# Optimization experiments

Measured on AMD Instinct MI355X. Metric: run time of the kernel, lower is better.

The kernel has to match this reference:

```python
import jax, jax.numpy as jnp
import numpy as np

D_MODEL = 1024
HEADS = 16


def setup_inputs() -> dict:
    key = jax.random.key(0)
    ks = jax.random.split(key, 11)
    B, S, D = 2, 2048, D_MODEL
    scale = 1.0 / np.sqrt(D)
    inp = {
        "q": jax.random.normal(ks[0], (B, S, D), jnp.float32),
        "k": jax.random.normal(ks[1], (B, S, D), jnp.float32),
        "v": jax.random.normal(ks[2], (B, S, D), jnp.float32),
        "w_q": jax.random.normal(ks[3], (D, D), jnp.float32) * scale,
        "b_q": jnp.zeros((D,), jnp.float32),
        "w_k": jax.random.normal(ks[4], (D, D), jnp.float32) * scale,
        "b_k": jnp.zeros((D,), jnp.float32),
        "w_v": jax.random.normal(ks[5], (D, D), jnp.float32) * scale,
        "b_v": jnp.zeros((D,), jnp.float32),
        "w_o": jax.random.normal(ks[6], (D, D), jnp.float32) * scale,
        "b_o": jnp.zeros((D,), jnp.float32),
    }
    return inp


def reference(q, k, v, w_q, b_q, w_k, b_k, w_v, b_v, w_o, b_o):
    B, S, D = q.shape
    H = HEADS
    Dh = D // H

    def split(x):  # [B,S,D] -> [B,H,S,Dh]
        return x.reshape(B, S, H, Dh).transpose(0, 2, 1, 3)

    qh = split(q @ w_q + b_q)
    kh = split(k @ w_k + b_k)
    vh = split(v @ w_v + b_v)

    # scaled dot-product attention: softmax(Q K^T / sqrt(Dh)) V
    scores = jnp.einsum("bhsd,bhtd->bhst", qh, kh) / jnp.sqrt(
        jnp.asarray(Dh, qh.dtype)
    )
    attn = jax.nn.softmax(scores, axis=-1)
    out = jnp.einsum("bhst,bhtd->bhsd", attn, vh)

    concat = out.transpose(0, 2, 1, 3).reshape(B, S, D)
    return concat @ w_o + b_o
```

## Files before the change

### kernel.cpp

```cpp
#include <hip/hip_runtime.h>
#include <hip/hip_bf16.h>
#include <math.h>

using bf16 = __hip_bfloat16;
typedef __bf16 bf16x8v __attribute__((ext_vector_type(8)));
typedef float f32x4v __attribute__((ext_vector_type(4)));

#define AS1 __attribute__((address_space(1)))
#define AS3 __attribute__((address_space(3)))

__device__ __forceinline__ void g2l16(const void* g, void* l) {
  __builtin_amdgcn_global_load_lds((const AS1 void*)g, (AS3 void*)l, 16, 0, 0);
}

__device__ __forceinline__ float fclamp(float v) {
  return fminf(fmaxf(v, -6.0e4f), 6.0e4f);
}

__device__ __forceinline__ unsigned packbf(float a, float b) {
  unsigned short lo = __builtin_bit_cast(unsigned short, __float2bfloat16(a));
  unsigned short hi = __builtin_bit_cast(unsigned short, __float2bfloat16(b));
  return (unsigned)lo | ((unsigned)hi << 16);
}

#define QSCL 0.1803368801111204f

__global__ __launch_bounds__(256) void transpose_cvt4(
    const float* __restrict__ w0, const float* __restrict__ w1,
    const float* __restrict__ w2, const float* __restrict__ w3,
    bf16* __restrict__ o0, bf16* __restrict__ o1,
    bf16* __restrict__ o2, bf16* __restrict__ o3) {
  const float* in = (blockIdx.z == 0) ? w0 : (blockIdx.z == 1) ? w1
                    : (blockIdx.z == 2) ? w2 : w3;
  bf16* out = (blockIdx.z == 0) ? o0 : (blockIdx.z == 1) ? o1
              : (blockIdx.z == 2) ? o2 : o3;
  __shared__ alignas(16) bf16 tile[64][80];
  const int t = threadIdx.x;
  const int bx = blockIdx.x * 64, by = blockIdx.y * 64;
#pragma unroll
  for (int p = 0; p < 4; ++p) {
    int idx = p * 1024 + t * 4;
    int r = idx >> 6, c0 = idx & 63;
    float4 v = *(const float4*)&in[(size_t)(by + r) * 1024 + bx + c0];
    tile[c0 + 0][r] = __float2bfloat16(v.x);
    tile[c0 + 1][r] = __float2bfloat16(v.y);
    tile[c0 + 2][r] = __float2bfloat16(v.z);
    tile[c0 + 3][r] = __float2bfloat16(v.w);
  }
  __syncthreads();
#pragma unroll
  for (int p = 0; p < 2; ++p) {
    int idx = p * 2048 + t * 8;
    int c = idx >> 6, r0 = idx & 63;
    *(uint4*)&out[(size_t)(bx + c) * 1024 + by + r0] = *(const uint4*)&tile[c][r0];
  }
}

__global__ __launch_bounds__(256) void cvt3(
    const float* __restrict__ q, const float* __restrict__ k,
    const float* __restrict__ v, bf16* __restrict__ oq,
    bf16* __restrict__ ok, bf16* __restrict__ ov) {
  const float* in = (blockIdx.y == 0) ? q : (blockIdx.y == 1) ? k : v;
  bf16* out = (blockIdx.y == 0) ? oq : (blockIdx.y == 1) ? ok : ov;
  int i = (blockIdx.x * 256 + threadIdx.x) * 8;
  float4 a = *(const float4*)&in[i];
  float4 b = *(const float4*)&in[i + 4];
  uint4 u;
  u.x = packbf(a.x, a.y); u.y = packbf(a.z, a.w);
  u.z = packbf(b.x, b.y); u.w = packbf(b.z, b.w);
  *(uint4*)&out[i] = u;
}

__global__ __launch_bounds__(256, 2) void gemm_qkv_bf16(
    const bf16* __restrict__ Aq, const bf16* __restrict__ Ak,
    const bf16* __restrict__ Av,
    const bf16* __restrict__ WtQ, const bf16* __restrict__ WtK,
    const bf16* __restrict__ WtV,
    const float* __restrict__ bq, const float* __restrict__ bk_,
    const float* __restrict__ bv_,
    bf16* __restrict__ Qh, bf16* __restrict__ Kh, bf16* __restrict__ Vt) {
  constexpr int K = 1024;
  const int z = blockIdx.z;
  const bf16* A    = (z == 0) ? Aq : (z == 1) ? Ak : Av;
  const bf16* Bt   = (z == 0) ? WtQ : (z == 1) ? WtK : WtV;
  const float* bias = (z == 0) ? bq : (z == 1) ? bk_ : bv_;
  bf16* C = (z == 0) ? Qh : (z == 1) ? Kh : Vt;

  __shared__ alignas(16) bf16 As[3][128 * 32];
  __shared__ alignas(16) bf16 Bs[3][128 * 32];
  const int t = threadIdx.x;
  const int wave = t >> 6, lane = t & 63;
  const int quad = lane >> 4, l16 = lane & 15;
  const int bm = blockIdx.x * 128, bn = blockIdx.y * 128;
  const int wm = (wave & 1) * 64, wn = (wave >> 1) * 64;

  f32x4v acc[4][4] = {};

  auto stage = [&](int ks, int buf) {
    int k0 = ks * 32;
#pragma unroll
    for (int c = 0; c < 2; ++c) {
      int idx = c * 2048 + t * 8;
      int row = idx >> 5, col = idx & 31;
      g2l16(&A[(size_t)(bm + row) * K + k0 + col], &As[buf][c * 2048 + wave * 512]);
      g2l16(&Bt[(size_t)(bn + row) * K + k0 + col], &Bs[buf][c * 2048 + wave * 512]);
    }
  };

  auto compute = [&](int buf) {
    bf16x8v a[4], b[4];
#pragma unroll
    for (int mi = 0; mi < 4; ++mi)
      a[mi] = *(const bf16x8v*)&As[buf][(wm + mi * 16 + l16) * 32 + quad * 8];
#pragma unroll
    for (int ni = 0; ni < 4; ++ni)
      b[ni] = *(const bf16x8v*)&Bs[buf][(wn + ni * 16 + l16) * 32 + quad * 8];
#pragma unroll
    for (int mi = 0; mi < 4; ++mi)
#pragma unroll
      for (int ni = 0; ni < 4; ++ni)
        acc[mi][ni] = __builtin_amdgcn_mfma_f32_16x16x32_bf16(a[mi], b[ni],
                                                              acc[mi][ni], 0, 0, 0);
  };

  stage(0, 0);
  asm volatile("s_waitcnt vmcnt(0)" ::: "memory");
  __builtin_amdgcn_s_barrier();
  stage(1, 1);

  int bufc = 0;
  for (int tt = 0; tt < 30; ++tt) {
    int bufs = bufc + 2; if (bufs >= 3) bufs -= 3;
    stage(tt + 2, bufs);
    compute(bufc);
    asm volatile("s_waitcnt vmcnt(4)" ::: "memory");
    __builtin_amdgcn_s_barrier();
    bufc = (bufc == 2) ? 0 : bufc + 1;
  }
  compute(bufc);
  asm volatile("s_waitcnt vmcnt(0)" ::: "memory");
  __builtin_amdgcn_s_barrier();
  bufc = (bufc == 2) ? 0 : bufc + 1;
  compute(bufc);

  if (z == 2) {
#pragma unroll
    for (int ni = 0; ni < 4; ++ni) {
      int n = bn + wn + ni * 16 + l16;
      float bz = bias[n];
      int h_ = n >> 6, d_ = n & 63;
#pragma unroll
      for (int mi = 0; mi < 4; ++mi) {
        int m0 = bm + wm + mi * 16 + quad * 4;
        int b_ = m0 >> 11, s0 = m0 & 2047;
        uint2 u;
        u.x = packbf(fclamp(acc[mi][ni][0] + bz), fclamp(acc[mi][ni][1] + bz));
        u.y = packbf(fclamp(acc[mi][ni][2] + bz), fclamp(acc[mi][ni][3] + bz));
        *(uint2*)&C[((size_t)(b_ * 16 + h_) * 64 + d_) * 2048 + s0] = u;
      }
    }
  } else {
    const float scl = (z == 0) ? QSCL : 1.0f;
#pragma unroll
    for (int ni = 0; ni < 4; ++ni) {
      int n = bn + wn + ni * 16 + l16;
      float bz = bias[n];
      int h_ = n >> 6, d_ = n & 63;
#pragma unroll
      for (int mi = 0; mi < 4; ++mi)
#pragma unroll
        for (int r = 0; r < 4; ++r) {
          int m = bm + wm + mi * 16 + quad * 4 + r;
          int b_ = m >> 11, s_ = m & 2047;
          C[((size_t)(b_ * 16 + h_) * 2048 + s_) * 64 + d_] =
              __float2bfloat16(fclamp(acc[mi][ni][r] + bz) * scl);
        }
    }
  }
}

__global__ __launch_bounds__(256, 2) void gemm_out(
    const bf16* __restrict__ A, const bf16* __restrict__ Bt,
    const float* __restrict__ bias, float* __restrict__ C) {
  constexpr int K = 1024, N = 1024;
  __shared__ alignas(16) bf16 As[3][128 * 32];
  __shared__ alignas(16) bf16 Bs[3][64 * 32];
  const int t = threadIdx.x;
  const int wave = t >> 6, lane = t & 63;
  const int quad = lane >> 4, l16 = lane & 15;
  const int bm = blockIdx.x * 128, bn = blockIdx.y * 64;
  const int wm = (wave & 1) * 64, wn = (wave >> 1) * 32;

  f32x4v acc[4][2] = {};

  auto stage = [&](int ks, int buf) {
    int k0 = ks * 32;
#pragma unroll
    for (int c = 0; c < 2; ++c) {
      int idx = c * 2048 + t * 8;
      int row = idx >> 5, col = idx & 31;
      g2l16(&A[(size_t)(bm + row) * K + k0 + col], &As[buf][c * 2048 + wave * 512]);
    }
    {
      int idx = t * 8;
      int row = idx >> 5, col = idx & 31;
      g2l16(&Bt[(size_t)(bn + row) * K + k0 + col], &Bs[buf][wave * 512]);
    }
  };

  auto compute = [&](int buf) {
    bf16x8v a[4], b[2];
#pragma unroll
    for (int mi = 0; mi < 4; ++mi)
      a[mi] = *(const bf16x8v*)&As[buf][(wm + mi * 16 + l16) * 32 + quad * 8];
#pragma unroll
    for (int ni = 0; ni < 2; ++ni)
      b[ni] = *(const bf16x8v*)&Bs[buf][(wn + ni * 16 + l16) * 32 + quad * 8];
#pragma unroll
    for (int mi = 0; mi < 4; ++mi)
#pragma unroll
      for (int ni = 0; ni < 2; ++ni)
        acc[mi][ni] = __builtin_amdgcn_mfma_f32_16x16x32_bf16(a[mi], b[ni],
                                                              acc[mi][ni], 0, 0, 0);
  };

  stage(0, 0);
  asm volatile("s_waitcnt vmcnt(0)" ::: "memory");
  __builtin_amdgcn_s_barrier();
  stage(1, 1);

  int bufc = 0;
  for (int tt = 0; tt < 30; ++tt) {
    int bufs = bufc + 2; if (bufs >= 3) bufs -= 3;
    stage(tt + 2, bufs);
    compute(bufc);
    asm volatile("s_waitcnt vmcnt(3)" ::: "memory");
    __builtin_amdgcn_s_barrier();
    bufc = (bufc == 2) ? 0 : bufc + 1;
  }
  compute(bufc);
  asm volatile("s_waitcnt vmcnt(0)" ::: "memory");
  __builtin_amdgcn_s_barrier();
  bufc = (bufc == 2) ? 0 : bufc + 1;
  compute(bufc);

#pragma unroll
  for (int ni = 0; ni < 2; ++ni) {
    int n = bn + wn + ni * 16 + l16;
    float bz = bias[n];
#pragma unroll
    for (int mi = 0; mi < 4; ++mi)
#pragma unroll
      for (int r = 0; r < 4; ++r) {
        int m = bm + wm + mi * 16 + quad * 4 + r;
        C[(size_t)m * N + n] = fclamp(acc[mi][ni][r] + bz);
      }
  }
}

__global__ __launch_bounds__(512, 4) void attn(
    const bf16* __restrict__ Qh, const bf16* __restrict__ Kh,
    const bf16* __restrict__ Vt, bf16* __restrict__ Ctx) {
  constexpr int LDPP = 40;
  __shared__ alignas(16) bf16 QsPs[128 * 64];
  __shared__ alignas(16) bf16 Ks[3][64 * 64];
  __shared__ alignas(16) bf16 Vs[3][64 * 64];
  const int t = threadIdx.x;
  const int wave = t >> 6, lane = t & 63;
  const int quad = lane >> 4, l16 = lane & 15;
  const int sw = l16 & 7;

  const int lin = blockIdx.x;
  const int li = lin >> 3;
  const int qb = li & 15;
  const int bh = (lin & 7) * 4 + (li >> 4);

  const size_t bh_off = (size_t)bh * 2048 * 64;
  const bf16* Qb = Qh + bh_off;
  const bf16* Kb = Kh + bh_off;
  const bf16* Vb = Vt + bh_off;

  const int srow = t >> 3;
  const int schunk = t & 7;

  auto stageKV = [&](int kt, int buf) {
    int mc = schunk ^ (srow & 7);
    g2l16(&Kb[(size_t)(kt * 64 + srow) * 64 + mc * 8], &Ks[buf][wave * 512]);
    g2l16(&Vb[(size_t)srow * 2048 + kt * 64 + mc * 8], &Vs[buf][wave * 512]);
  };

#pragma unroll
  for (int c = 0; c < 2; ++c) {
    int row = c * 64 + srow;
    int mc = schunk ^ (row & 7);
    g2l16(&Qb[(size_t)(qb * 128 + row) * 64 + mc * 8],
          &QsPs[c * 4096 + wave * 512]);
  }
  stageKV(0, 0);
  asm volatile("s_waitcnt vmcnt(2)" ::: "memory");
  __builtin_amdgcn_s_barrier();

  bf16x8v aq[2];
#pragma unroll
  for (int kk = 0; kk < 2; ++kk)
    aq[kk] = *(const bf16x8v*)
        &QsPs[(wave * 16 + l16) * 64 + (((kk * 4 + quad) ^ sw) << 3)];

  __syncthreads();
  bf16* Psw = QsPs + wave * (16 * LDPP);

  stageKV(1, 1);

  bf16x8v vone;
#pragma unroll
  for (int i = 0; i < 8; ++i) vone[i] = (__bf16)1.0f;

  f32x4v lsum = {};
  f32x4v oacc[4] = {};

  auto compute = [&](int buf) {
#pragma unroll
    for (int h = 0; h < 2; ++h) {
      f32x4v s[2] = {};
      __builtin_amdgcn_s_setprio(1);
#pragma unroll
      for (int kk = 0; kk < 2; ++kk)
#pragma unroll
        for (int ni = 0; ni < 2; ++ni) {
          bf16x8v bk = *(const bf16x8v*)
              &Ks[buf][(h * 32 + ni * 16 + l16) * 64 + (((kk * 4 + quad) ^ sw) << 3)];
          s[ni] = __builtin_amdgcn_mfma_f32_16x16x32_bf16(bk, aq[kk],
                                                          s[ni], 0, 0, 0);
        }
      __builtin_amdgcn_s_setprio(0);

#pragma unroll
      for (int ni = 0; ni < 2; ++ni) {
        float p0 = __builtin_amdgcn_exp2f(fminf(s[ni][0], 80.f));
        float p1 = __builtin_amdgcn_exp2f(fminf(s[ni][1], 80.f));
        float p2 = __builtin_amdgcn_exp2f(fminf(s[ni][2], 80.f));
        float p3 = __builtin_amdgcn_exp2f(fminf(s[ni][3], 80.f));
        uint2 u;
        u.x = packbf(p0, p1);
        u.y = packbf(p2, p3);
        *(uint2*)&Psw[l16 * LDPP + ni * 16 + quad * 4] = u;
      }

      bf16x8v ap = *(const bf16x8v*)&Psw[l16 * LDPP + quad * 8];
      __builtin_amdgcn_s_setprio(1);
      lsum = __builtin_amdgcn_mfma_f32_16x16x32_bf16(ap, vone, lsum, 0, 0, 0);
#pragma unroll
      for (int ni = 0; ni < 4; ++ni) {
        bf16x8v bv = *(const bf16x8v*)
            &Vs[buf][(ni * 16 + l16) * 64 + (((h * 4 + quad) ^ sw) << 3)];
        oacc[ni] = __builtin_amdgcn_mfma_f32_16x16x32_bf16(ap, bv, oacc[ni],
                                                           0, 0, 0);
      }
      __builtin_amdgcn_s_setprio(0);
    }
  };

  int bufc = 0;
  for (int tt = 0; tt < 30; ++tt) {
    int bufs = bufc + 2; if (bufs >= 3) bufs -= 3;
    stageKV(tt + 2, bufs);
    compute(bufc);
    asm volatile("s_waitcnt vmcnt(2)" ::: "memory");
    __builtin_amdgcn_s_barrier();
    bufc = (bufc == 2) ? 0 : bufc + 1;
  }
  compute(bufc);
  asm volatile("s_waitcnt vmcnt(0)" ::: "memory");
  __builtin_amdgcn_s_barrier();
  bufc = (bufc == 2) ? 0 : bufc + 1;
  compute(bufc);

  const int b_ = bh >> 4, h_ = bh & 15;
#pragma unroll
  for (int r = 0; r < 4; ++r) {
    int sr = qb * 128 + wave * 16 + quad * 4 + r;
    float inv = 1.0f / fmaxf(lsum[r], 1.0e-20f);
#pragma unroll
    for (int ni = 0; ni < 4; ++ni) {
      int col = h_ * 64 + ni * 16 + l16;
      Ctx[(size_t)(b_ * 2048 + sr) * 1024 + col] =
          __float2bfloat16(fclamp(oacc[ni][r] * inv));
    }
  }
}

extern "C" void kernel_launch(void* const* d_in, const int* in_sizes, int n_in,
                              void* d_out, int out_size, void* d_ws, size_t ws_size,
                              hipStream_t stream) {
  const float* q   = (const float*)d_in[0];
  const float* k   = (const float*)d_in[1];
  const float* v   = (const float*)d_in[2];
  const float* w_q = (const float*)d_in[3];
  const float* b_q = (const float*)d_in[4];
  const float* w_k = (const float*)d_in[5];
  const float* b_k = (const float*)d_in[6];
  const float* w_v = (const float*)d_in[7];
  const float* b_v = (const float*)d_in[8];
  const float* w_o = (const float*)d_in[9];
  const float* b_o = (const float*)d_in[10];
  float* out = (float*)d_out;

  char* ws = (char*)d_ws;
  const size_t MB = (size_t)1024 * 1024;
  bf16* WtQ = (bf16*)(ws + 0 * MB);
  bf16* WtK = (bf16*)(ws + 2 * MB);
  bf16* WtV = (bf16*)(ws + 4 * MB);
  bf16* WtO = (bf16*)(ws + 6 * MB);
  bf16* Qa  = (bf16*)(ws + 8 * MB);
  bf16* Ka  = (bf16*)(ws + 16 * MB);
  bf16* Va  = (bf16*)(ws + 24 * MB);
  bf16* Qh  = (bf16*)(ws + 32 * MB);
  bf16* Kh  = (bf16*)(ws + 40 * MB);
  bf16* Vt  = (bf16*)(ws + 48 * MB);
  bf16* Ctx = Qa;

  dim3 tb(256);
  transpose_cvt4<<<dim3(16, 16, 4), tb, 0, stream>>>(w_q, w_k, w_v, w_o,
                                                     WtQ, WtK, WtV, WtO);
  cvt3<<<dim3(2048, 3), tb, 0, stream>>>(q, k, v, Qa, Ka, Va);
  gemm_qkv_bf16<<<dim3(32, 8, 3), tb, 0, stream>>>(Qa, Ka, Va, WtQ, WtK, WtV,
                                                   b_q, b_k, b_v, Qh, Kh, Vt);
  attn<<<dim3(512), dim3(512), 0, stream>>>(Qh, Kh, Vt, Ctx);
  gemm_out<<<dim3(32, 16), tb, 0, stream>>>(Ctx, WtO, b_o, out);
}
```

Measured before the change: 224.6 us.

## Merge conversion kernels and switch attention to 128-key double-buffered tiles

Fuses the weight transpose-convert and activation convert kernels into a single launch, saving one kernel launch. The attention kernel moves from a triple-buffered 64-key pipeline to a double-buffered pipeline with 128-key tiles. This halves the number of barriers and waits, but each wait is now vmcnt(0), so there is less prefetch depth. LDS use grows from 64KB to 80KB per block, which may reduce occupancy below the 4-block launch bound.

```diff
diff --git a/kernel.cpp b/kernel.cpp
--- a/kernel.cpp
+++ b/kernel.cpp
@@ -25,27 +25,44 @@
 
 #define QSCL 0.1803368801111204f
 
-__global__ __launch_bounds__(256) void transpose_cvt4(
+__global__ __launch_bounds__(256) void prep(
+    const float* __restrict__ q, const float* __restrict__ k,
+    const float* __restrict__ v,
     const float* __restrict__ w0, const float* __restrict__ w1,
     const float* __restrict__ w2, const float* __restrict__ w3,
+    bf16* __restrict__ oq, bf16* __restrict__ ok, bf16* __restrict__ ov,
     bf16* __restrict__ o0, bf16* __restrict__ o1,
     bf16* __restrict__ o2, bf16* __restrict__ o3) {
-  const float* in = (blockIdx.z == 0) ? w0 : (blockIdx.z == 1) ? w1
-                    : (blockIdx.z == 2) ? w2 : w3;
-  bf16* out = (blockIdx.z == 0) ? o0 : (blockIdx.z == 1) ? o1
-              : (blockIdx.z == 2) ? o2 : o3;
   __shared__ alignas(16) bf16 tile[64][80];
   const int t = threadIdx.x;
-  const int bx = blockIdx.x * 64, by = blockIdx.y * 64;
+  const int lin = blockIdx.x;
+  if (lin < 6144) {
+    const int tensor = lin >> 11, blk = lin & 2047;
+    const float* in = (tensor == 0) ? q : (tensor == 1) ? k : v;
+    bf16* out = (tensor == 0) ? oq : (tensor == 1) ? ok : ov;
+    int i = (blk * 256 + t) * 8;
+    float4 a = *(const float4*)&in[i];
+    float4 b = *(const float4*)&in[i + 4];
+    uint4 u;
+    u.x = packbf(a.x, a.y); u.y = packbf(a.z, a.w);
+    u.z = packbf(b.x, b.y); u.w = packbf(b.z, b.w);
+    *(uint4*)&out[i] = u;
+    return;
+  }
+  const int rem = lin - 6144;
+  const int z = rem >> 8, xy = rem & 255;
+  const float* in = (z == 0) ? w0 : (z == 1) ? w1 : (z == 2) ? w2 : w3;
+  bf16* out = (z == 0) ? o0 : (z == 1) ? o1 : (z == 2) ? o2 : o3;
+  const int bx = (xy & 15) * 64, by = (xy >> 4) * 64;
 #pragma unroll
   for (int p = 0; p < 4; ++p) {
     int idx = p * 1024 + t * 4;
     int r = idx >> 6, c0 = idx & 63;
-    float4 v = *(const float4*)&in[(size_t)(by + r) * 1024 + bx + c0];
-    tile[c0 + 0][r] = __float2bfloat16(v.x);
-    tile[c0 + 1][r] = __float2bfloat16(v.y);
-    tile[c0 + 2][r] = __float2bfloat16(v.z);
-    tile[c0 + 3][r] = __float2bfloat16(v.w);
+    float4 vv = *(const float4*)&in[(size_t)(by + r) * 1024 + bx + c0];
+    tile[c0 + 0][r] = __float2bfloat16(vv.x);
+    tile[c0 + 1][r] = __float2bfloat16(vv.y);
+    tile[c0 + 2][r] = __float2bfloat16(vv.z);
+    tile[c0 + 3][r] = __float2bfloat16(vv.w);
   }
   __syncthreads();
 #pragma unroll
@@ -54,21 +71,6 @@
     int c = idx >> 6, r0 = idx & 63;
     *(uint4*)&out[(size_t)(bx + c) * 1024 + by + r0] = *(const uint4*)&tile[c][r0];
   }
-}
-
-__global__ __launch_bounds__(256) void cvt3(
-    const float* __restrict__ q, const float* __restrict__ k,
-    const float* __restrict__ v, bf16* __restrict__ oq,
-    bf16* __restrict__ ok, bf16* __restrict__ ov) {
-  const float* in = (blockIdx.y == 0) ? q : (blockIdx.y == 1) ? k : v;
-  bf16* out = (blockIdx.y == 0) ? oq : (blockIdx.y == 1) ? ok : ov;
-  int i = (blockIdx.x * 256 + threadIdx.x) * 8;
-  float4 a = *(const float4*)&in[i];
-  float4 b = *(const float4*)&in[i + 4];
-  uint4 u;
-  u.x = packbf(a.x, a.y); u.y = packbf(a.z, a.w);
-  u.z = packbf(b.x, b.y); u.w = packbf(b.z, b.w);
-  *(uint4*)&out[i] = u;
 }
 
 __global__ __launch_bounds__(256, 2) void gemm_qkv_bf16(
@@ -263,8 +265,8 @@
     const bf16* __restrict__ Vt, bf16* __restrict__ Ctx) {
   constexpr int LDPP = 40;
   __shared__ alignas(16) bf16 QsPs[128 * 64];
-  __shared__ alignas(16) bf16 Ks[3][64 * 64];
-  __shared__ alignas(16) bf16 Vs[3][64 * 64];
+  __shared__ alignas(16) bf16 Ks[2][128 * 64];
+  __shared__ alignas(16) bf16 Vs[2][128 * 64];
   const int t = threadIdx.x;
   const int wave = t >> 6, lane = t & 63;
   const int quad = lane >> 4, l16 = lane & 15;
@@ -285,8 +287,13 @@
 
   auto stageKV = [&](int kt, int buf) {
     int mc = schunk ^ (srow & 7);
-    g2l16(&Kb[(size_t)(kt * 64 + srow) * 64 + mc * 8], &Ks[buf][wave * 512]);
-    g2l16(&Vb[(size_t)srow * 2048 + kt * 64 + mc * 8], &Vs[buf][wave * 512]);
+#pragma unroll
+    for (int c = 0; c < 2; ++c) {
+      g2l16(&Kb[(size_t)(kt * 128 + c * 64 + srow) * 64 + mc * 8],
+            &Ks[buf][c * 4096 + wave * 512]);
+      g2l16(&Vb[(size_t)srow * 2048 + kt * 128 + c * 64 + mc * 8],
+            &Vs[buf][c * 4096 + wave * 512]);
+    }
   };
 
 #pragma unroll
@@ -297,7 +304,7 @@
           &QsPs[c * 4096 + wave * 512]);
   }
   stageKV(0, 0);
-  asm volatile("s_waitcnt vmcnt(2)" ::: "memory");
+  asm volatile("s_waitcnt vmcnt(4)" ::: "memory");
   __builtin_amdgcn_s_barrier();
 
   bf16x8v aq[2];
@@ -309,8 +316,6 @@
   __syncthreads();
   bf16* Psw = QsPs + wave * (16 * LDPP);
 
-  stageKV(1, 1);
-
   bf16x8v vone;
 #pragma unroll
   for (int i = 0; i < 8; ++i) vone[i] = (__bf16)1.0f;
@@ -320,7 +325,8 @@
 
   auto compute = [&](int buf) {
 #pragma unroll
-    for (int h = 0; h < 2; ++h) {
+    for (int h = 0; h < 4; ++h) {
+      const int hc = h >> 1, hl = h & 1;
       f32x4v s[2] = {};
       __builtin_amdgcn_s_setprio(1);
 #pragma unroll
@@ -328,7 +334,8 @@
 #pragma unroll
         for (int ni = 0; ni < 2; ++ni) {
           bf16x8v bk = *(const bf16x8v*)
-              &Ks[buf][(h * 32 + ni * 16 + l16) * 64 + (((kk * 4 + quad) ^ sw) << 3)];
+              &Ks[buf][hc * 4096 + (hl * 32 + ni * 16 + l16) * 64 +
+                       (((kk * 4 + quad) ^ sw) << 3)];
           s[ni] = __builtin_amdgcn_mfma_f32_16x16x32_bf16(bk, aq[kk],
                                                           s[ni], 0, 0, 0);
         }
@@ -352,7 +359,8 @@
 #pragma unroll
       for (int ni = 0; ni < 4; ++ni) {
         bf16x8v bv = *(const bf16x8v*)
-            &Vs[buf][(ni * 16 + l16) * 64 + (((h * 4 + quad) ^ sw) << 3)];
+            &Vs[buf][hc * 4096 + (ni * 16 + l16) * 64 +
+                     (((hl * 4 + quad) ^ sw) << 3)];
         oacc[ni] = __builtin_amdgcn_mfma_f32_16x16x32_bf16(ap, bv, oacc[ni],
                                                            0, 0, 0);
       }
@@ -360,20 +368,14 @@
     }
   };
 
-  int bufc = 0;
-  for (int tt = 0; tt < 30; ++tt) {
-    int bufs = bufc + 2; if (bufs >= 3) bufs -= 3;
-    stageKV(tt + 2, bufs);
-    compute(bufc);
-    asm volatile("s_waitcnt vmcnt(2)" ::: "memory");
-    __builtin_amdgcn_s_barrier();
-    bufc = (bufc == 2) ? 0 : bufc + 1;
-  }
-  compute(bufc);
-  asm volatile("s_waitcnt vmcnt(0)" ::: "memory");
-  __builtin_amdgcn_s_barrier();
-  bufc = (bufc == 2) ? 0 : bufc + 1;
-  compute(bufc);
+  for (int tt = 0; tt < 16; ++tt) {
+    if (tt + 1 < 16) stageKV(tt + 1, (tt + 1) & 1);
+    compute(tt & 1);
+    if (tt + 1 < 16) {
+      asm volatile("s_waitcnt vmcnt(0)" ::: "memory");
+      __builtin_amdgcn_s_barrier();
+    }
+  }
 
   const int b_ = bh >> 4, h_ = bh & 15;
 #pragma unroll
@@ -420,9 +422,8 @@
   bf16* Ctx = Qa;
 
   dim3 tb(256);
-  transpose_cvt4<<<dim3(16, 16, 4), tb, 0, stream>>>(w_q, w_k, w_v, w_o,
-                                                     WtQ, WtK, WtV, WtO);
-  cvt3<<<dim3(2048, 3), tb, 0, stream>>>(q, k, v, Qa, Ka, Va);
+  prep<<<dim3(7168), tb, 0, stream>>>(q, k, v, w_q, w_k, w_v, w_o,
+                                      Qa, Ka, Va, WtQ, WtK, WtV, WtO);
   gemm_qkv_bf16<<<dim3(32, 8, 3), tb, 0, stream>>>(Qa, Ka, Va, WtQ, WtK, WtV,
                                                    b_q, b_k, b_v, Qh, Kh, Vt);
   attn<<<dim3(512), dim3(512), 0, stream>>>(Qh, Kh, Vt, Ctx);
```

Result: no change. 223.8 us (-0.3%).
